# Optimization experiments

Measured on AMD Instinct MI355X. Metric: run time of the kernel, lower is better.

Reference implementation:

```python
import jax, jax.numpy as jnp
import numpy as np

V_TH = 1.0  # spikingjelly IFNode default threshold; v starts at 0, hard reset after fire


def setup_inputs() -> dict:
    key = jax.random.key(0)
    k_x, k_w1, k_w2 = jax.random.split(key, 3)
    B, IN, FEAT, OUT = 4096, 3136, 6272, 500
    # binary input spikes (LatencyEncoder emits 0/1 spikes per timestep)
    x = (jax.random.uniform(k_x, (B, IN)) < 0.5).astype(jnp.float32)
    # Linear weights, torch layout [out_features, in_features], kaiming-ish scale
    W1 = jax.random.normal(k_w1, (FEAT, IN), dtype=jnp.float32) / np.sqrt(IN)
    W2 = jax.random.normal(k_w2, (OUT, FEAT), dtype=jnp.float32) / np.sqrt(FEAT)
    return {"x": x, "W1": W1, "W2": W2}


def reference(x, W1, W2):
    # Linear (no bias) -> IF neuron single step: v = 0 + I; spike = (v >= V_TH); hard reset
    v1 = x @ W1.T                      # [B, FEAT]
    s1 = (v1 >= V_TH).astype(x.dtype)  # binary hidden spikes
    v2 = s1 @ W2.T                     # [B, OUT]
    s2 = (v2 >= V_TH).astype(x.dtype)  # output spikes
    return s2
```

## Files before the change

kernel.cpp:

```cpp
#include <hip/hip_runtime.h>


namespace {
constexpr int kB = 4096;
constexpr int kIn = 3136;
constexpr int kFeat = 6272;
constexpr int kFeatWords = 196;
constexpr int kOut = 500;
constexpr size_t kPlane1 = (size_t)kFeat * kIn;
constexpr size_t kW1F = 3 * kPlane1;
constexpr size_t kW2F = (size_t)784 * 12288;
constexpr size_t kS1Bytes = (size_t)kB * kFeatWords * 4;
constexpr size_t kXb2Bytes = (size_t)49 * kB * 8;
constexpr unsigned kCap1 = 1u << 20;
constexpr unsigned kCap2 = 1u << 16;
__device__ constexpr double kTau1 = 7.4769e-4;
__device__ constexpr double kTau2 = 1.4955e-3;
}

typedef int v4i __attribute__((ext_vector_type(4)));
typedef int v16i __attribute__((ext_vector_type(16)));

__device__ __forceinline__ v4i expand16(unsigned b) {
  unsigned u0 = (((b      ) & 0xFu) * 0x204081u) & 0x01010101u;
  unsigned u1 = (((b >> 4 ) & 0xFu) * 0x204081u) & 0x01010101u;
  unsigned u2 = (((b >> 8 ) & 0xFu) * 0x204081u) & 0x01010101u;
  unsigned u3 = (((b >> 12) & 0xFu) * 0x204081u) & 0x01010101u;
  return (v4i){(int)u0, (int)u1, (int)u2, (int)u3};
}

__device__ __forceinline__ void split3(float w, signed char* d) {
  float c = rintf(w * 128.f);
  d[0] = (signed char)(int)c;
  float r = fmaf(c, -7.8125e-03f, w);
  c = rintf(r * 16384.f);
  d[1] = (signed char)(int)c;
  r = fmaf(c, -6.103515625e-05f, r);
  c = rintf(r * 2097152.f);
  d[2] = (signed char)(int)c;
}

__global__ __launch_bounds__(256) void conv_w1F(const float* __restrict__ W,
                                                signed char* __restrict__ F) {
  const int bx = blockIdx.x;
  const int fb = bx / 49;
  const int kt = bx % 49;
  const int f = threadIdx.x & 63;
  const int g = threadIdx.x >> 6;
  const float* src = W + (size_t)(fb * 64 + f) * kIn + kt * 64 + g * 16;
  union { signed char c[16]; int4 v; } o[3];
#pragma unroll
  for (int q = 0; q < 4; ++q) {
    const float4 w = *(const float4*)(src + q * 4);
    signed char d[4][3];
    split3(w.x, d[0]); split3(w.y, d[1]); split3(w.z, d[2]); split3(w.w, d[3]);
#pragma unroll
    for (int e = 0; e < 4; ++e)
#pragma unroll
      for (int j = 0; j < 3; ++j) o[j].c[q * 4 + e] = d[e][j];
  }
#pragma unroll
  for (int j = 0; j < 3; ++j)
    *(int4*)(F + ((size_t)bx * 3 + j) * 4096 + g * 1024 + f * 16) = o[j].v;
}

__global__ __launch_bounds__(256) void conv_w2F(const float* __restrict__ W,
                                                signed char* __restrict__ F) {
  const int bx = blockIdx.x;
  const int fb = bx / 98;
  const int kt = bx % 98;
  const int f = threadIdx.x & 63;
  const int g = threadIdx.x >> 6;
  const int feat = fb * 64 + f;
  union { signed char c[16]; int4 v; } o[3];
#pragma unroll
  for (int q = 0; q < 4; ++q) {
    float4 w = {0.f, 0.f, 0.f, 0.f};
    if (feat < kOut)
      w = *(const float4*)(W + (size_t)feat * kFeat + kt * 64 + g * 16 + q * 4);
    signed char d[4][3];
    split3(w.x, d[0]); split3(w.y, d[1]); split3(w.z, d[2]); split3(w.w, d[3]);
#pragma unroll
    for (int e = 0; e < 4; ++e)
#pragma unroll
      for (int j = 0; j < 3; ++j) o[j].c[q * 4 + e] = d[e][j];
  }
#pragma unroll
  for (int j = 0; j < 3; ++j)
    *(int4*)(F + ((size_t)bx * 3 + j) * 4096 + g * 1024 + f * 16) = o[j].v;
}

__global__ __launch_bounds__(256) void pack_x2(const float* __restrict__ X,
                                               uint2* __restrict__ xb2) {
  const int wid = (blockIdx.x * 256 + threadIdx.x) >> 6;
  const int lane = threadIdx.x & 63;
  const int b = wid / 49;
  const int g = wid % 49;
  const float v = X[(size_t)b * kIn + g * 64 + lane];
  const unsigned long long bal = __ballot(v != 0.f);
  if (lane == 0) xb2[(size_t)g * kB + b] = make_uint2((unsigned)bal, (unsigned)(bal >> 32));
}

__global__ __launch_bounds__(128, 2) void fc1_v13(
    const uint2* __restrict__ xb2, const signed char* __restrict__ w1lF,
    unsigned* __restrict__ s1b, unsigned* __restrict__ s1T,
    unsigned* __restrict__ cnt, unsigned* __restrict__ list) {
  const int tid = threadIdx.x;
  const int lane = tid & 63;
  const int ln31 = lane & 31;
  const int half = lane >> 5;
  const int wvN = tid >> 6;

  const int lin = blockIdx.x + 32 * blockIdx.y;
  const int sw = (lin & 7) * 392 + (lin >> 3);
  const int bx = sw >> 5;
  const int bM = (sw & 31) * 128;

  const signed char* const gb = w1lF + (size_t)bx * 49 * 12288;
  const unsigned hsel = half * 1024u + (wvN * 32 + ln31) * 16u;
  const uint2* const aptr = xb2 + bM + ln31;

  v16i acc[4][3] = {};
  v4i b0[3], b1[3];
  uint2 aC[4], aN[4];

#define FC1_LB(KT, KK, BF)                                                    \
  {                                                                           \
    const signed char* bp_ = gb + (size_t)(KT) * 12288 + (KK) * 2048 + hsel;  \
    (BF)[0] = *(const v4i*)(bp_);                                             \
    (BF)[1] = *(const v4i*)(bp_ + 4096);                                      \
    (BF)[2] = *(const v4i*)(bp_ + 8192);                                      \
  }
#define FC1_LA(KT, AR)                                                        \
  {                                                                           \
    _Pragma("unroll")                                                         \
    for (int s = 0; s < 4; ++s) (AR)[s] = aptr[(size_t)(KT) * kB + s * 32];   \
  }
#define FC1_COMP(BF, AW, SEL)                                                 \
  {                                                                           \
    _Pragma("unroll")                                                         \
    for (int s = 0; s < 4; ++s) {                                             \
      const unsigned w_ = (SEL) ? (AW)[s].y : (AW)[s].x;                      \
      const v4i a_ = expand16((w_ >> (half * 16)) & 0xFFFFu);                 \
      acc[s][0] = __builtin_amdgcn_mfma_i32_32x32x32_i8(a_, (BF)[0], acc[s][0], 0, 0, 0); \
      acc[s][1] = __builtin_amdgcn_mfma_i32_32x32x32_i8(a_, (BF)[1], acc[s][1], 0, 0, 0); \
      acc[s][2] = __builtin_amdgcn_mfma_i32_32x32x32_i8(a_, (BF)[2], acc[s][2], 0, 0, 0); \
    }                                                                         \
  }

  FC1_LB(0, 0, b0);
  FC1_LA(0, aC);
#pragma unroll
  for (int s = 0; s < 4; ++s) aN[s] = aC[s];

  for (int kt = 0; kt < 49; ++kt) {
    FC1_LB(kt, 1, b1);
    if (kt < 48) FC1_LA(kt + 1, aN);
    FC1_COMP(b0, aC, 0);
    if (kt < 48) FC1_LB(kt + 1, 0, b0);
    FC1_COMP(b1, aC, 1);
#pragma unroll
    for (int s = 0; s < 4; ++s) aC[s] = aN[s];
  }
#undef FC1_LB
#undef FC1_LA
#undef FC1_COMP

  const double s7 = 0.0078125;
  const int word = bx * 2 + wvN;
  const int fcol = word * 32 + ln31;
#pragma unroll
  for (int sub = 0; sub < 4; ++sub) {
#pragma unroll
    for (int t = 0; t < 16; ++t) {
      double v = (double)acc[sub][2][t];
      v = v * s7 + (double)acc[sub][1][t];
      v = v * s7 + (double)acc[sub][0][t];
      v = v * s7;
      const unsigned long long bal = __ballot(v >= 1.0);
      const int mrow = bM + sub * 32 + (t & 3) + 8 * (t >> 2);
      if (lane == 0) {
        s1b[(size_t)mrow * kFeatWords + word] = (unsigned)bal;
        s1T[(size_t)word * kB + mrow] = (unsigned)bal;
      }
      if (lane == 32) {
        s1b[(size_t)(mrow + 4) * kFeatWords + word] = (unsigned)(bal >> 32);
        s1T[(size_t)word * kB + mrow + 4] = (unsigned)(bal >> 32);
      }
      if (fabs(v - 1.0) <= kTau1) {
        const unsigned idx = atomicAdd(cnt, 1u);
        if (idx < kCap1) list[idx] = ((unsigned)(mrow + 4 * half) << 13) | (unsigned)fcol;
      }
    }
  }
}

__global__ __launch_bounds__(256) void fc1_correct(
    const float* __restrict__ x, const float* __restrict__ W1,
    const unsigned* __restrict__ cnt, const unsigned* __restrict__ list,
    unsigned* __restrict__ s1b, unsigned* __restrict__ s1T) {
  const unsigned n = min(cnt[0], kCap1);
  const int lane = threadIdx.x & 63;
  const int wid = (blockIdx.x * 256 + threadIdx.x) >> 6;
  const int nw = (gridDim.x * 256) >> 6;
  for (unsigned i = wid; i < n; i += nw) {
    const unsigned u = list[i];
    const int b = (int)(u >> 13);
    const int f = (int)(u & 8191u);
    double s = 0.0;
    for (int k = lane; k < kIn; k += 64)
      s = fma((double)x[(size_t)b * kIn + k], (double)W1[(size_t)f * kIn + k], s);
#pragma unroll
    for (int off = 32; off > 0; off >>= 1) s += __shfl_down(s, off);
    if (lane == 0) {
      const unsigned mask = 1u << (f & 31);
      unsigned* p1 = s1b + (size_t)b * kFeatWords + (f >> 5);
      unsigned* p2 = s1T + (size_t)(f >> 5) * kB + b;
      if (s >= 1.0) { atomicOr(p1, mask); atomicOr(p2, mask); }
      else          { atomicAnd(p1, ~mask); atomicAnd(p2, ~mask); }
    }
  }
}

__global__ __launch_bounds__(128, 4) void fc2_v7(
    const unsigned* __restrict__ s1T, const signed char* __restrict__ w2lF,
    float* __restrict__ out, unsigned* __restrict__ cnt,
    unsigned* __restrict__ list) {
  const int tid = threadIdx.x;
  const int lane = tid & 63;
  const int ln31 = lane & 31;
  const int half = lane >> 5;
  const int wvN = tid >> 6;

  const int lin = blockIdx.x + 128 * blockIdx.y;
  const int sw = ((lin & 7) << 7) + (lin >> 3);
  const int bx = sw >> 7;
  const int bM = (sw & 127) * 32;

  const unsigned* const aptr = s1T + bM + ln31;
  const int fl = wvN * 32 + ln31;
  const signed char* const bbase =
      w2lF + (size_t)(bx * 98) * 12288 + half * 1024u + fl * 16u;

  v16i acc[3] = {};
  v4i b0[6], b1[6];
  uint2 a0, a1;

#define LOAD_TILE(nk, bf, ab)                                   \
  {                                                             \
    const signed char* bp = bbase + (size_t)(nk) * 12288;       \
    bf[0] = *(const v4i*)(bp);                                  \
    bf[1] = *(const v4i*)(bp + 2048);                           \
    bf[2] = *(const v4i*)(bp + 4096);                           \
    bf[3] = *(const v4i*)(bp + 6144);                           \
    bf[4] = *(const v4i*)(bp + 8192);                           \
    bf[5] = *(const v4i*)(bp + 10240);                          \
    (ab).x = aptr[(size_t)((nk) * 2) * kB];                     \
    (ab).y = aptr[(size_t)((nk) * 2 + 1) * kB];                 \
  }
#define COMPUTE_TILE(bf, ab)                                                    \
  {                                                                             \
    _Pragma("unroll")                                                           \
    for (int kk = 0; kk < 2; ++kk) {                                            \
      const unsigned word = kk ? (ab).y : (ab).x;                               \
      const v4i a = expand16((word >> (half * 16)) & 0xFFFFu);                  \
      acc[0] = __builtin_amdgcn_mfma_i32_32x32x32_i8(a, bf[kk], acc[0], 0,0,0); \
      acc[1] = __builtin_amdgcn_mfma_i32_32x32x32_i8(a, bf[2+kk], acc[1],0,0,0);\
      acc[2] = __builtin_amdgcn_mfma_i32_32x32x32_i8(a, bf[4+kk], acc[2],0,0,0);\
    }                                                                           \
  }

  LOAD_TILE(0, b0, a0);
  for (int kt = 0; kt + 2 <= 98; kt += 2) {
    LOAD_TILE(kt + 1, b1, a1);
    COMPUTE_TILE(b0, a0);
    const int nk2 = (kt + 2 < 98) ? kt + 2 : 97;
    LOAD_TILE(nk2, b0, a0);
    COMPUTE_TILE(b1, a1);
  }

  const double s7 = 0.0078125;
  const int o = bx * 64 + wvN * 32 + ln31;
#pragma unroll
  for (int t = 0; t < 16; ++t) {
    double v = (double)acc[2][t];
    v = v * s7 + (double)acc[1][t];
    v = v * s7 + (double)acc[0][t];
    v = v * s7;
    const int b = bM + (t & 3) + 8 * (t >> 2) + 4 * half;
    if (o < kOut) {
      out[(size_t)b * kOut + o] = (v >= 1.0) ? 1.0f : 0.0f;
      if (fabs(v - 1.0) <= kTau2) {
        const unsigned idx = atomicAdd(cnt, 1u);
        if (idx < kCap2) list[idx] = ((unsigned)b << 13) | (unsigned)o;
      }
    }
  }
#undef LOAD_TILE
#undef COMPUTE_TILE
}

__global__ __launch_bounds__(256) void fc2_correct(
    const unsigned* __restrict__ s1b, const float* __restrict__ W2,
    const unsigned* __restrict__ cnt, const unsigned* __restrict__ list,
    float* __restrict__ out) {
  const unsigned n = min(cnt[0], kCap2);
  const int lane = threadIdx.x & 63;
  const int wid = (blockIdx.x * 256 + threadIdx.x) >> 6;
  const int nw = (gridDim.x * 256) >> 6;
  for (unsigned i = wid; i < n; i += nw) {
    const unsigned u = list[i];
    const int b = (int)(u >> 13);
    const int o = (int)(u & 8191u);
    double s = 0.0;
    for (int k = lane; k < kFeat; k += 64) {
      const unsigned w = s1b[(size_t)b * kFeatWords + (k >> 5)];
      if ((w >> (k & 31)) & 1u) s += (double)W2[(size_t)o * kFeat + k];
    }
#pragma unroll
    for (int off = 32; off > 0; off >>= 1) s += __shfl_down(s, off);
    if (lane == 0) out[(size_t)b * kOut + o] = (s >= 1.0) ? 1.0f : 0.0f;
  }
}

__global__ __launch_bounds__(256) void snn_fc1(const float* __restrict__ x,
                                               const float* __restrict__ W1,
                                               unsigned int* __restrict__ s1bits) {
  __shared__ double Xd[32][66];
  __shared__ double Wd[32][66];
  __shared__ unsigned int spikes[64][2];
  const int tid = threadIdx.x;
  const int tx = tid & 15;
  const int ty = tid >> 4;
  const int b0 = blockIdx.y * 64;
  const int f0 = blockIdx.x * 64;
  if (tid < 128) spikes[tid >> 1][tid & 1] = 0u;
  double acc[4][4];
#pragma unroll
  for (int j = 0; j < 4; ++j)
#pragma unroll
    for (int i = 0; i < 4; ++i) acc[j][i] = 0.0;
  const int rl = tid >> 2;
  const int kq = (tid & 3) * 8;
  const float* xrow = x + (size_t)(b0 + rl) * kIn + kq;
  const float* wrow = W1 + (size_t)(f0 + rl) * kIn + kq;
  for (int kc = 0; kc < kIn; kc += 32) {
    const float4 xv0 = *(const float4*)(xrow + kc);
    const float4 xv1 = *(const float4*)(xrow + kc + 4);
    const float4 wv0 = *(const float4*)(wrow + kc);
    const float4 wv1 = *(const float4*)(wrow + kc + 4);
    __syncthreads();
    Xd[kq + 0][rl] = (double)xv0.x; Xd[kq + 1][rl] = (double)xv0.y;
    Xd[kq + 2][rl] = (double)xv0.z; Xd[kq + 3][rl] = (double)xv0.w;
    Xd[kq + 4][rl] = (double)xv1.x; Xd[kq + 5][rl] = (double)xv1.y;
    Xd[kq + 6][rl] = (double)xv1.z; Xd[kq + 7][rl] = (double)xv1.w;
    Wd[kq + 0][rl] = (double)wv0.x; Wd[kq + 1][rl] = (double)wv0.y;
    Wd[kq + 2][rl] = (double)wv0.z; Wd[kq + 3][rl] = (double)wv0.w;
    Wd[kq + 4][rl] = (double)wv1.x; Wd[kq + 5][rl] = (double)wv1.y;
    Wd[kq + 6][rl] = (double)wv1.z; Wd[kq + 7][rl] = (double)wv1.w;
    __syncthreads();
#pragma unroll
    for (int k = 0; k < 32; ++k) {
      const double2 xa = *(const double2*)&Xd[k][ty * 4];
      const double2 xb = *(const double2*)&Xd[k][ty * 4 + 2];
      const double2 wa = *(const double2*)&Wd[k][tx * 4];
      const double2 wb = *(const double2*)&Wd[k][tx * 4 + 2];
      const double xv[4] = {xa.x, xa.y, xb.x, xb.y};
      const double wv[4] = {wa.x, wa.y, wb.x, wb.y};
#pragma unroll
      for (int j = 0; j < 4; ++j)
#pragma unroll
        for (int i = 0; i < 4; ++i) acc[j][i] += xv[j] * wv[i];
    }
  }
  __syncthreads();
#pragma unroll
  for (int j = 0; j < 4; ++j) {
    unsigned int nib = 0u;
#pragma unroll
    for (int i = 0; i < 4; ++i) nib |= (acc[j][i] >= 1.0 ? 1u : 0u) << i;
    atomicOr(&spikes[ty * 4 + j][tx >> 3], nib << ((tx * 4) & 31));
  }
  __syncthreads();
  if (tid < 128) {
    const int r = tid >> 1;
    const int w = tid & 1;
    s1bits[(size_t)(b0 + r) * kFeatWords + (f0 >> 5) + w] = spikes[r][w];
  }
}

__global__ __launch_bounds__(256) void snn_fc2(const unsigned int* __restrict__ s1bits,
                                               const float* __restrict__ W2,
                                               float* __restrict__ out) {
  __shared__ double Wd[32][66];
  __shared__ unsigned int Sb[64];
  const int tid = threadIdx.x;
  const int tx = tid & 15;
  const int ty = tid >> 4;
  const int b0 = blockIdx.y * 64;
  const int o0 = blockIdx.x * 64;
  double acc[4][4];
#pragma unroll
  for (int j = 0; j < 4; ++j)
#pragma unroll
    for (int i = 0; i < 4; ++i) acc[j][i] = 0.0;
  const int rl = tid >> 2;
  const int kq = (tid & 3) * 8;
  int orow = o0 + rl;
  if (orow >= kOut) orow = kOut - 1;
  const float* wrow = W2 + (size_t)orow * kFeat + kq;
  for (int kc = 0; kc < kFeat; kc += 32) {
    const float4 wv0 = *(const float4*)(wrow + kc);
    const float4 wv1 = *(const float4*)(wrow + kc + 4);
    unsigned int sword = 0u;
    if (tid < 64) sword = s1bits[(size_t)(b0 + tid) * kFeatWords + (kc >> 5)];
    __syncthreads();
    Wd[kq + 0][rl] = (double)wv0.x; Wd[kq + 1][rl] = (double)wv0.y;
    Wd[kq + 2][rl] = (double)wv0.z; Wd[kq + 3][rl] = (double)wv0.w;
    Wd[kq + 4][rl] = (double)wv1.x; Wd[kq + 5][rl] = (double)wv1.y;
    Wd[kq + 6][rl] = (double)wv1.z; Wd[kq + 7][rl] = (double)wv1.w;
    if (tid < 64) Sb[tid] = sword;
    __syncthreads();
    const unsigned int rw0 = Sb[ty * 4 + 0];
    const unsigned int rw1 = Sb[ty * 4 + 1];
    const unsigned int rw2 = Sb[ty * 4 + 2];
    const unsigned int rw3 = Sb[ty * 4 + 3];
#pragma unroll
    for (int k = 0; k < 32; ++k) {
      const double2 wa = *(const double2*)&Wd[k][tx * 4];
      const double2 wb = *(const double2*)&Wd[k][tx * 4 + 2];
      const double wv[4] = {wa.x, wa.y, wb.x, wb.y};
      const double sv[4] = {(double)((rw0 >> k) & 1u), (double)((rw1 >> k) & 1u),
                            (double)((rw2 >> k) & 1u), (double)((rw3 >> k) & 1u)};
#pragma unroll
      for (int j = 0; j < 4; ++j)
#pragma unroll
        for (int i = 0; i < 4; ++i) acc[j][i] += sv[j] * wv[i];
    }
  }
#pragma unroll
  for (int j = 0; j < 4; ++j) {
    const int b = b0 + ty * 4 + j;
#pragma unroll
    for (int i = 0; i < 4; ++i) {
      const int o = o0 + tx * 4 + i;
      if (o < kOut) out[(size_t)b * kOut + o] = (acc[j][i] >= 1.0) ? 1.0f : 0.0f;
    }
  }
}

extern "C" void kernel_launch(void* const* d_in, const int* in_sizes, int n_in,
                              void* d_out, int out_size, void* d_ws, size_t ws_size,
                              hipStream_t stream) {
  const float* x = (const float*)d_in[0];
  const float* W1 = (const float*)d_in[1];
  const float* W2 = (const float*)d_in[2];
  float* out = (float*)d_out;

  char* p = (char*)d_ws;
  signed char* w1lF = (signed char*)p;   p += kW1F;
  signed char* w2lF = (signed char*)p;   p += kW2F;
  unsigned* s1b = (unsigned*)p;          p += kS1Bytes;
  unsigned* s1T = (unsigned*)p;          p += kS1Bytes;
  uint2* xb2 = (uint2*)p;                p += kXb2Bytes;
  unsigned* list1 = (unsigned*)p;        p += (size_t)kCap1 * 4;
  unsigned* list2 = (unsigned*)p;        p += (size_t)kCap2 * 4;
  unsigned* ctrs = (unsigned*)p;         p += 256;
  const size_t need = (size_t)(p - (char*)d_ws);

  if (ws_size >= need) {
    hipMemsetAsync(ctrs, 0, 32, stream);
    conv_w1F<<<4802, 256, 0, stream>>>(W1, w1lF);
    conv_w2F<<<784, 256, 0, stream>>>(W2, w2lF);
    pack_x2<<<50176, 256, 0, stream>>>(x, xb2);
    fc1_v13<<<dim3(32, 98), 128, 0, stream>>>(xb2, w1lF, s1b, s1T, ctrs, list1);
    fc1_correct<<<1024, 256, 0, stream>>>(x, W1, ctrs, list1, s1b, s1T);
    fc2_v7<<<dim3(128, 8), 128, 0, stream>>>(s1T, w2lF, out, ctrs + 4, list2);
    fc2_correct<<<64, 256, 0, stream>>>(s1b, W2, ctrs + 4, list2, out);
  } else {
    unsigned* s1 = (unsigned*)d_ws;
    snn_fc1<<<dim3(98, 64), 256, 0, stream>>>(x, W1, s1);
    snn_fc2<<<dim3(8, 64), 256, 0, stream>>>(s1, W2, out);
  }
}
```

Before: 564.9 us.

## Shrink fc1 tiles to single-wave 64x32 blocks with setprio and unrolled pipeline

The fc1 kernel moves from 128-thread blocks that compute a 128x64 output tile to single-wave blocks that compute a 64x32 tile, which quadruples the grid. The K loop is unrolled by two with incremental pointer advances, and each MFMA group is wrapped in s_setprio. The aim is more waves for latency hiding and less address arithmetic. In exchange, each block loads its A and B operands with less reuse, which raises global and L2 traffic.

```diff
diff --git a/kernel.cpp b/kernel.cpp
--- a/kernel.cpp
+++ b/kernel.cpp
@@ -101,76 +101,82 @@
   if (lane == 0) xb2[(size_t)g * kB + b] = make_uint2((unsigned)bal, (unsigned)(bal >> 32));
 }
 
-__global__ __launch_bounds__(128, 2) void fc1_v13(
+__global__ __launch_bounds__(64, 3) void fc1_v14(
     const uint2* __restrict__ xb2, const signed char* __restrict__ w1lF,
     unsigned* __restrict__ s1b, unsigned* __restrict__ s1T,
     unsigned* __restrict__ cnt, unsigned* __restrict__ list) {
-  const int tid = threadIdx.x;
-  const int lane = tid & 63;
+  const int lane = threadIdx.x & 63;
   const int ln31 = lane & 31;
   const int half = lane >> 5;
-  const int wvN = tid >> 6;
-
-  const int lin = blockIdx.x + 32 * blockIdx.y;
-  const int sw = (lin & 7) * 392 + (lin >> 3);
-  const int bx = sw >> 5;
-  const int bM = (sw & 31) * 128;
-
-  const signed char* const gb = w1lF + (size_t)bx * 49 * 12288;
-  const unsigned hsel = half * 1024u + (wvN * 32 + ln31) * 16u;
-  const uint2* const aptr = xb2 + bM + ln31;
-
-  v16i acc[4][3] = {};
+
+  const int lin = blockIdx.x + 64 * blockIdx.y;
+  const int sw = (lin & 7) * 1568 + (lin >> 3);
+  const int m = sw & 63;
+  const int p32 = sw >> 6;
+  const int fb64 = p32 >> 1;
+  const int nh = p32 & 1;
+  const int bM = m * 64;
+
+  const signed char* const gb = w1lF + (size_t)fb64 * 49 * 12288;
+  const unsigned hsel = half * 1024u + (nh * 32 + ln31) * 16u;
+  const uint2* ap = xb2 + bM + ln31;
+  const signed char* bp = gb + hsel;
+
+  v16i acc[2][3] = {};
   v4i b0[3], b1[3];
-  uint2 aC[4], aN[4];
-
-#define FC1_LB(KT, KK, BF)                                                    \
+  uint2 aC0, aC1, aN0, aN1;
+
+#define FC1_LB(PTR, KK, BF)                                                   \
   {                                                                           \
-    const signed char* bp_ = gb + (size_t)(KT) * 12288 + (KK) * 2048 + hsel;  \
-    (BF)[0] = *(const v4i*)(bp_);                                             \
-    (BF)[1] = *(const v4i*)(bp_ + 4096);                                      \
-    (BF)[2] = *(const v4i*)(bp_ + 8192);                                      \
-  }
-#define FC1_LA(KT, AR)                                                        \
+    (BF)[0] = *(const v4i*)((PTR) + (KK) * 2048);                             \
+    (BF)[1] = *(const v4i*)((PTR) + (KK) * 2048 + 4096);                      \
+    (BF)[2] = *(const v4i*)((PTR) + (KK) * 2048 + 8192);                      \
+  }
+#define FC1_COMP2(BF, W0, W1)                                                 \
   {                                                                           \
-    _Pragma("unroll")                                                         \
-    for (int s = 0; s < 4; ++s) (AR)[s] = aptr[(size_t)(KT) * kB + s * 32];   \
-  }
-#define FC1_COMP(BF, AW, SEL)                                                 \
-  {                                                                           \
-    _Pragma("unroll")                                                         \
-    for (int s = 0; s < 4; ++s) {                                             \
-      const unsigned w_ = (SEL) ? (AW)[s].y : (AW)[s].x;                      \
-      const v4i a_ = expand16((w_ >> (half * 16)) & 0xFFFFu);                 \
-      acc[s][0] = __builtin_amdgcn_mfma_i32_32x32x32_i8(a_, (BF)[0], acc[s][0], 0, 0, 0); \
-      acc[s][1] = __builtin_amdgcn_mfma_i32_32x32x32_i8(a_, (BF)[1], acc[s][1], 0, 0, 0); \
-      acc[s][2] = __builtin_amdgcn_mfma_i32_32x32x32_i8(a_, (BF)[2], acc[s][2], 0, 0, 0); \
-    }                                                                         \
-  }
-
-  FC1_LB(0, 0, b0);
-  FC1_LA(0, aC);
-#pragma unroll
-  for (int s = 0; s < 4; ++s) aN[s] = aC[s];
-
-  for (int kt = 0; kt < 49; ++kt) {
-    FC1_LB(kt, 1, b1);
-    if (kt < 48) FC1_LA(kt + 1, aN);
-    FC1_COMP(b0, aC, 0);
-    if (kt < 48) FC1_LB(kt + 1, 0, b0);
-    FC1_COMP(b1, aC, 1);
-#pragma unroll
-    for (int s = 0; s < 4; ++s) aC[s] = aN[s];
-  }
+    const v4i a0_ = expand16(((W0) >> (half * 16)) & 0xFFFFu);                \
+    const v4i a1_ = expand16(((W1) >> (half * 16)) & 0xFFFFu);                \
+    __builtin_amdgcn_s_setprio(1);                                            \
+    acc[0][0] = __builtin_amdgcn_mfma_i32_32x32x32_i8(a0_, (BF)[0], acc[0][0], 0, 0, 0); \
+    acc[0][1] = __builtin_amdgcn_mfma_i32_32x32x32_i8(a0_, (BF)[1], acc[0][1], 0, 0, 0); \
+    acc[0][2] = __builtin_amdgcn_mfma_i32_32x32x32_i8(a0_, (BF)[2], acc[0][2], 0, 0, 0); \
+    acc[1][0] = __builtin_amdgcn_mfma_i32_32x32x32_i8(a1_, (BF)[0], acc[1][0], 0, 0, 0); \
+    acc[1][1] = __builtin_amdgcn_mfma_i32_32x32x32_i8(a1_, (BF)[1], acc[1][1], 0, 0, 0); \
+    acc[1][2] = __builtin_amdgcn_mfma_i32_32x32x32_i8(a1_, (BF)[2], acc[1][2], 0, 0, 0); \
+    __builtin_amdgcn_s_setprio(0);                                            \
+  }
+
+  FC1_LB(bp, 0, b0);
+  aC0 = ap[0];
+  aC1 = ap[32];
+
+  for (int t = 0; t < 24; ++t) {
+    FC1_LB(bp, 1, b1);
+    aN0 = ap[kB]; aN1 = ap[kB + 32];
+    FC1_COMP2(b0, aC0.x, aC1.x);
+    bp += 12288;
+    FC1_LB(bp, 0, b0);
+    FC1_COMP2(b1, aC0.y, aC1.y);
+    ap += kB;
+    FC1_LB(bp, 1, b1);
+    aC0 = ap[kB]; aC1 = ap[kB + 32];
+    FC1_COMP2(b0, aN0.x, aN1.x);
+    bp += 12288;
+    FC1_LB(bp, 0, b0);
+    FC1_COMP2(b1, aN0.y, aN1.y);
+    ap += kB;
+  }
+  FC1_LB(bp, 1, b1);
+  FC1_COMP2(b0, aC0.x, aC1.x);
+  FC1_COMP2(b1, aC0.y, aC1.y);
 #undef FC1_LB
-#undef FC1_LA
-#undef FC1_COMP
+#undef FC1_COMP2
 
   const double s7 = 0.0078125;
-  const int word = bx * 2 + wvN;
-  const int fcol = word * 32 + ln31;
-#pragma unroll
-  for (int sub = 0; sub < 4; ++sub) {
+  const int word = p32;
+  const int fcol = p32 * 32 + ln31;
+#pragma unroll
+  for (int sub = 0; sub < 2; ++sub) {
 #pragma unroll
     for (int t = 0; t < 16; ++t) {
       double v = (double)acc[sub][2][t];
@@ -473,7 +479,7 @@
     conv_w1F<<<4802, 256, 0, stream>>>(W1, w1lF);
     conv_w2F<<<784, 256, 0, stream>>>(W2, w2lF);
     pack_x2<<<50176, 256, 0, stream>>>(x, xb2);
-    fc1_v13<<<dim3(32, 98), 128, 0, stream>>>(xb2, w1lF, s1b, s1T, ctrs, list1);
+    fc1_v14<<<dim3(64, 196), 64, 0, stream>>>(xb2, w1lF, s1b, s1T, ctrs, list1);
     fc1_correct<<<1024, 256, 0, stream>>>(x, W1, ctrs, list1, s1b, s1T);
     fc2_v7<<<dim3(128, 8), 128, 0, stream>>>(s1T, w2lF, out, ctrs + 4, list2);
     fc2_correct<<<64, 256, 0, stream>>>(s1b, W2, ctrs + 4, list2, out);
```

After: 571.5 us. About the same (+1.2%).
